# Kernel tuning notes

Hardware: AMD Instinct MI355X
Metric: run time of the kernel (lower is better)

Reference implementation:

```python
import jax, jax.numpy as jnp
import numpy as np

B, S, D = 8, 2048, 512

def setup_inputs() -> dict:
    key = jax.random.key(0)
    ks = jax.random.split(key, 9)
    scale = 1.0 / np.sqrt(D)
    return {
        "x": jax.random.normal(ks[0], (B, S, D), dtype=jnp.float32),
        "attention_mask": jax.random.uniform(ks[1], (B, S), dtype=jnp.float32),
        "Wq": jax.random.normal(ks[2], (D, D), dtype=jnp.float32) * scale,
        "bq": jax.random.normal(ks[3], (D,), dtype=jnp.float32) * 0.01,
        "Wk": jax.random.normal(ks[4], (D, D), dtype=jnp.float32) * scale,
        "bk": jax.random.normal(ks[5], (D,), dtype=jnp.float32) * 0.01,
        "Wv": jax.random.normal(ks[6], (D, D), dtype=jnp.float32) * scale,
        "bv": jax.random.normal(ks[7], (D,), dtype=jnp.float32) * 0.01,
    }

def reference(x, attention_mask, Wq, bq, Wk, bk, Wv, bv):
    # Single-head self-attention, full O(S^2) scores as in the original.
    q = jnp.einsum('bsd,df->bsf', x, Wq) + bq  # [B,S,D]
    k = jnp.einsum('bsd,df->bsf', x, Wk) + bk
    v = jnp.einsum('bsd,df->bsf', x, Wv) + bv
    scores = jnp.einsum('bqd,bkd->bqk', q, k) / jnp.sqrt(jnp.float32(D))  # [B,S,S]
    attn = jax.nn.softmax(scores, axis=2)
    weighted = jnp.einsum('bqk,bkd->bqd', attn, v)  # [B,S,D]
    # mask applied multiplicatively to the output, per original code
    return weighted * attention_mask[:, :, None]
```

## Files before the change

kernel.cpp:

```cpp
#include <hip/hip_runtime.h>
#include <math.h>
#include <stdint.h>


typedef _Float16 f16x8 __attribute__((ext_vector_type(8)));
typedef _Float16 f16x4 __attribute__((ext_vector_type(4)));
typedef _Float16 f16x2 __attribute__((ext_vector_type(2)));
typedef float f32x4 __attribute__((ext_vector_type(4)));

__device__ __forceinline__ void async16(const _Float16* g, _Float16* l) {
    __builtin_amdgcn_global_load_lds(
        (const __attribute__((address_space(1))) unsigned int*)(uintptr_t)g,
        (__attribute__((address_space(3))) unsigned int*)(unsigned int)(uintptr_t)l,
        16, 0, 0);
}

__device__ __forceinline__ float frag_sum8(f16x8 v, float acc) {
#if __has_builtin(__builtin_amdgcn_fdot2)
    const f16x2 one2 = {(_Float16)1.f, (_Float16)1.f};
    const f16x2* p = (const f16x2*)&v;
    acc = __builtin_amdgcn_fdot2(p[0], one2, acc, false);
    acc = __builtin_amdgcn_fdot2(p[1], one2, acc, false);
    acc = __builtin_amdgcn_fdot2(p[2], one2, acc, false);
    acc = __builtin_amdgcn_fdot2(p[3], one2, acc, false);
#else
#pragma unroll
    for (int j = 0; j < 8; j++) acc += (float)v[j];
#endif
    return acc;
}

template <bool WITH_RS>
__device__ __forceinline__ void mfma_gemm_core64(
    const _Float16* __restrict__ A, int lda,
    const _Float16* __restrict__ B, int ldb,
    int K, int row0, int col0,
    _Float16* As, _Float16* Bs, f32x4 acc[4][4], float rs[4])
{
    const int tid  = threadIdx.x;
    const int lane = tid & 63;
    const int wave = tid >> 6;
    const int wm   = wave >> 1, wn = wave & 1;

    const int rc  = lane >> 3;
    const int swz = ((lane & 7) ^ rc) * 8;

    const _Float16* gA[4]; const _Float16* gB[4];
    _Float16* lA[4]; _Float16* lB[4];
#pragma unroll
    for (int i = 0; i < 4; i++) {
        int c = wave * 4 + i;
        gA[i] = A + (size_t)(row0 + 8 * c + rc) * lda + swz;
        gB[i] = B + (size_t)(col0 + 8 * c + rc) * ldb + swz;
        lA[i] = As + c * 512;
        lB[i] = Bs + c * 512;
    }

    const int fr = lane & 15;
    const int q  = lane >> 4;
    const int fx = fr & 7;

    for (int k0 = 0; k0 < K; k0 += 64) {
        __syncthreads();
#pragma unroll
        for (int i = 0; i < 4; i++) {
            async16(gA[i] + k0, lA[i]);
            async16(gB[i] + k0, lB[i]);
        }
        __syncthreads();
#pragma unroll
        for (int step = 0; step < 2; step++) {
            f16x8 af[4], bf[4];
#pragma unroll
            for (int t = 0; t < 4; t++) {
                int ra = wm * 64 + t * 16 + fr;
                int rb = wn * 64 + t * 16 + fr;
                int kc = ((step * 4 + q) ^ fx) * 8;
                af[t] = *(const f16x8*)&As[ra * 64 + kc];
                bf[t] = *(const f16x8*)&Bs[rb * 64 + kc];
            }
            if (WITH_RS) {
#pragma unroll
                for (int t = 0; t < 4; t++) rs[t] = frag_sum8(af[t], rs[t]);
            }
#pragma unroll
            for (int tm = 0; tm < 4; tm++)
#pragma unroll
                for (int tn = 0; tn < 4; tn++)
                    acc[tm][tn] = __builtin_amdgcn_mfma_f32_16x16x32_f16(
                        af[tm], bf[tn], acc[tm][tn], 0, 0, 0);
        }
    }
}

__global__ __launch_bounds__(256) void prep(
    const float* __restrict__ x,
    const float* __restrict__ Wq, const float* __restrict__ Wk,
    const float* __restrict__ Wv,
    _Float16* __restrict__ Xh,
    _Float16* __restrict__ WqT, _Float16* __restrict__ WkT,
    _Float16* __restrict__ WvT)
{
    const int bid = blockIdx.x;
    if (bid < 8192) {
        int i = (bid * 256 + threadIdx.x) * 4;
        float4 v = *(const float4*)(x + i);
        f16x4 h;
        h.x = (_Float16)v.x; h.y = (_Float16)v.y;
        h.z = (_Float16)v.z; h.w = (_Float16)v.w;
        *(f16x4*)&Xh[i] = h;
    } else {
        int t = bid - 8192;
        int z = t >> 10;
        const float* W = (z == 0) ? Wq : (z == 1) ? Wk : Wv;
        _Float16* Wt   = (z == 0) ? WqT : (z == 1) ? WkT : WvT;
        int idx = (t & 1023) * 256 + threadIdx.x;
        int n = idx >> 9, k = idx & 511;
        Wt[idx] = (_Float16)W[k * 512 + n];
    }
}

__global__ __launch_bounds__(256) void proj_mfma(
    const _Float16* __restrict__ Xh,
    const _Float16* __restrict__ WqT, const float* __restrict__ bq,
    const _Float16* __restrict__ WkT, const float* __restrict__ bk,
    const _Float16* __restrict__ WvT, const float* __restrict__ bv,
    _Float16* __restrict__ Qh, _Float16* __restrict__ Kh,
    _Float16* __restrict__ Vt)
{
    __shared__ __align__(16) _Float16 smem[2 * 128 * 64];
    _Float16* As = smem;
    _Float16* Bs = smem + 128 * 64;

    const int z = blockIdx.z;
    f32x4 acc[4][4];
#pragma unroll
    for (int i = 0; i < 4; i++)
#pragma unroll
        for (int j = 0; j < 4; j++) acc[i][j] = (f32x4){0.f, 0.f, 0.f, 0.f};
    float rs_unused[4];

    const int lane = threadIdx.x & 63, wave = threadIdx.x >> 6;
    const int wm = wave >> 1, wn = wave & 1;
    const int er = (lane >> 4) * 4, ec = lane & 15;

    if (z < 2) {
        const _Float16* Wt = (z == 0) ? WqT : WkT;
        const float* bias  = (z == 0) ? bq : bk;
        _Float16* P        = (z == 0) ? Qh : Kh;
        const float sc     = (z == 0) ? 0.04419417382415922f : 1.0f;
        const int row0 = blockIdx.x * 128, col0 = blockIdx.y * 128;
        mfma_gemm_core64<false>(Xh, 512, Wt, 512, 512, row0, col0, As, Bs, acc,
                                rs_unused);
#pragma unroll
        for (int tm = 0; tm < 4; tm++)
#pragma unroll
            for (int tn = 0; tn < 4; tn++) {
                int col = col0 + wn * 64 + tn * 16 + ec;
                float bb = bias[col];
#pragma unroll
                for (int r = 0; r < 4; r++) {
                    int row = row0 + wm * 64 + tm * 16 + er + r;
                    P[(size_t)row * 512 + col] = (_Float16)((acc[tm][tn][r] + bb) * sc);
                }
            }
    } else {
        const int row0 = blockIdx.y * 128;
        const int col0 = blockIdx.x * 128;
        mfma_gemm_core64<false>(WvT, 512, Xh, 512, 512, row0, col0, As, Bs, acc,
                                rs_unused);
#pragma unroll
        for (int tm = 0; tm < 4; tm++)
#pragma unroll
            for (int tn = 0; tn < 4; tn++) {
                int col = col0 + wn * 64 + tn * 16 + ec;
                size_t obase = (size_t)(col >> 11) * (512 * 2048) + (col & 2047);
#pragma unroll
                for (int r = 0; r < 4; r++) {
                    int row = row0 + wm * 64 + tm * 16 + er + r;
                    Vt[obase + (size_t)row * 2048] = (_Float16)(acc[tm][tn][r] + bv[row]);
                }
            }
    }
}

__global__ __launch_bounds__(256) void scores_mfma(
    const _Float16* __restrict__ Qh, const _Float16* __restrict__ Kh,
    _Float16* __restrict__ Sh)
{
    __shared__ __align__(16) _Float16 smem[2 * 128 * 64];
    _Float16* As = smem;
    _Float16* Bs = smem + 128 * 64;
    const int bid = blockIdx.x;
    const int b   = bid & 7;
    const int rem = bid >> 3;
    const int col0 = (rem & 15) * 128;
    const int row0 = (rem >> 4) * 128;

    const _Float16* A = Qh + (size_t)b * 2048 * 512;
    const _Float16* B = Kh + (size_t)b * 2048 * 512;
    _Float16* S = Sh + (size_t)b * 2048 * 2048;

    f32x4 acc[4][4];
#pragma unroll
    for (int i = 0; i < 4; i++)
#pragma unroll
        for (int j = 0; j < 4; j++) acc[i][j] = (f32x4){0.f, 0.f, 0.f, 0.f};
    float rs_unused[4];

    mfma_gemm_core64<false>(A, 512, B, 512, 512, row0, col0, As, Bs, acc,
                            rs_unused);

    const int lane = threadIdx.x & 63, wave = threadIdx.x >> 6;
    const int wm = wave >> 1, wn = wave & 1;
    const int er = (lane >> 4) * 4, ec = lane & 15;
#pragma unroll
    for (int tm = 0; tm < 4; tm++)
#pragma unroll
        for (int tn = 0; tn < 4; tn++) {
            int col = col0 + wn * 64 + tn * 16 + ec;
#pragma unroll
            for (int r = 0; r < 4; r++) {
                int row = row0 + wm * 64 + tm * 16 + er + r;
                S[(size_t)row * 2048 + col] = (_Float16)__expf(acc[tm][tn][r]);
            }
        }
}

__global__ __launch_bounds__(256) void av_mfma(
    const _Float16* __restrict__ Sh, const _Float16* __restrict__ Vt,
    const float* __restrict__ mask, float* __restrict__ out)
{
    __shared__ __align__(16) _Float16 smem[2 * 128 * 64];
    __shared__ float l_s[128];
    _Float16* As = smem;
    _Float16* Bs = smem + 128 * 64;
    const int bid = blockIdx.x;
    const int b   = bid & 7;
    const int rem = bid >> 3;
    const int col0 = (rem & 3) * 128;
    const int row0 = (rem >> 2) * 128;

    const _Float16* A = Sh + (size_t)b * 2048 * 2048;
    const _Float16* B = Vt + (size_t)b * 512 * 2048;
    float* O = out + (size_t)b * 2048 * 512;
    const float* mk = mask + (size_t)b * 2048;

    f32x4 acc[4][4];
#pragma unroll
    for (int i = 0; i < 4; i++)
#pragma unroll
        for (int j = 0; j < 4; j++) acc[i][j] = (f32x4){0.f, 0.f, 0.f, 0.f};
    float rs[4] = {0.f, 0.f, 0.f, 0.f};

    mfma_gemm_core64<true>(A, 2048, B, 2048, 2048, row0, col0, As, Bs, acc, rs);

    const int lane = threadIdx.x & 63, wave = threadIdx.x >> 6;
    const int wm = wave >> 1, wn = wave & 1;
    const int er = (lane >> 4) * 4, ec = lane & 15;

#pragma unroll
    for (int t = 0; t < 4; t++) {
        rs[t] += __shfl_xor(rs[t], 16, 64);
        rs[t] += __shfl_xor(rs[t], 32, 64);
    }
    if (wn == 0 && lane < 16) {
#pragma unroll
        for (int t = 0; t < 4; t++) l_s[wm * 64 + t * 16 + lane] = rs[t];
    }
    __syncthreads();

#pragma unroll
    for (int tm = 0; tm < 4; tm++)
#pragma unroll
        for (int r = 0; r < 4; r++) {
            int lrow = wm * 64 + tm * 16 + er + r;
            int row = row0 + lrow;
            float s = mk[row] / l_s[lrow];
#pragma unroll
            for (int tn = 0; tn < 4; tn++) {
                int col = col0 + wn * 64 + tn * 16 + ec;
                O[(size_t)row * 512 + col] = acc[tm][tn][r] * s;
            }
        }
}

extern "C" void kernel_launch(void* const* d_in, const int* in_sizes, int n_in,
                              void* d_out, int out_size, void* d_ws, size_t ws_size,
                              hipStream_t stream) {
    const float* x    = (const float*)d_in[0];
    const float* mask = (const float*)d_in[1];
    const float* Wq   = (const float*)d_in[2];
    const float* bq   = (const float*)d_in[3];
    const float* Wk   = (const float*)d_in[4];
    const float* bk   = (const float*)d_in[5];
    const float* Wv   = (const float*)d_in[6];
    const float* bv   = (const float*)d_in[7];
    float* out = (float*)d_out;

    const size_t BSD = (size_t)8 * 2048 * 512;
    _Float16* base = (_Float16*)d_ws;
    _Float16* Qh  = base;
    _Float16* Kh  = Qh + BSD;
    _Float16* Vt  = Kh + BSD;
    _Float16* WqT = Vt + BSD;
    _Float16* WkT = WqT + 512 * 512;
    _Float16* WvT = WkT + 512 * 512;
    _Float16* Xh  = WvT + 512 * 512;
    _Float16* Sh  = Xh;

    dim3 blk(256);
    prep<<<dim3(8192 + 3 * 1024), blk, 0, stream>>>(
        x, Wq, Wk, Wv, Xh, WqT, WkT, WvT);
    proj_mfma<<<dim3(128, 4, 3), blk, 0, stream>>>(
        Xh, WqT, bq, WkT, bk, WvT, bv, Qh, Kh, Vt);
    scores_mfma<<<dim3(2048), blk, 0, stream>>>(Qh, Kh, Sh);
    av_mfma<<<dim3(512), blk, 0, stream>>>(Sh, Vt, mask, out);
}
```

Baseline: 220.8 us.

## Double-buffer LDS tiles in MFMA GEMM core to overlap loads with compute

The shared GEMM core now uses two LDS buffers, issuing async global-to-LDS loads for the next K tile before computing on the current one, and waits with explicit vmcnt counts instead of full syncthreads. LDS per block doubles to 64 KB, and l_s in av_mfma reuses the tile buffer after an added barrier. This hides global load latency behind the MFMA work in all three GEMM kernels, at the cost of halving how many blocks fit per CU in LDS and relying on hand-placed waitcnt and barriers being correct.

```diff
diff --git a/kernel.cpp b/kernel.cpp
--- a/kernel.cpp
+++ b/kernel.cpp
@@ -35,7 +35,7 @@
     const _Float16* __restrict__ A, int lda,
     const _Float16* __restrict__ B, int ldb,
     int K, int row0, int col0,
-    _Float16* As, _Float16* Bs, f32x4 acc[4][4], float rs[4])
+    _Float16* sm, f32x4 acc[4][4], float rs[4])
 {
     const int tid  = threadIdx.x;
     const int lane = tid & 63;
@@ -46,28 +46,45 @@
     const int swz = ((lane & 7) ^ rc) * 8;
 
     const _Float16* gA[4]; const _Float16* gB[4];
-    _Float16* lA[4]; _Float16* lB[4];
+    int lA[4], lB[4];
 #pragma unroll
     for (int i = 0; i < 4; i++) {
         int c = wave * 4 + i;
         gA[i] = A + (size_t)(row0 + 8 * c + rc) * lda + swz;
         gB[i] = B + (size_t)(col0 + 8 * c + rc) * ldb + swz;
-        lA[i] = As + c * 512;
-        lB[i] = Bs + c * 512;
+        lA[i] = c * 512;
+        lB[i] = 8192 + c * 512;
     }
 
     const int fr = lane & 15;
     const int q  = lane >> 4;
     const int fx = fr & 7;
 
-    for (int k0 = 0; k0 < K; k0 += 64) {
-        __syncthreads();
-#pragma unroll
-        for (int i = 0; i < 4; i++) {
-            async16(gA[i] + k0, lA[i]);
-            async16(gB[i] + k0, lB[i]);
+#pragma unroll
+    for (int i = 0; i < 4; i++) {
+        async16(gA[i], sm + lA[i]);
+        async16(gB[i], sm + lB[i]);
+    }
+
+    int cur = 0;
+    for (int k0 = 0;; k0 += 64) {
+        const bool more = (k0 + 64) < K;
+        if (more) {
+            const int nb = (cur ^ 1) * 16384;
+#pragma unroll
+            for (int i = 0; i < 4; i++) {
+                async16(gA[i] + k0 + 64, sm + nb + lA[i]);
+                async16(gB[i] + k0 + 64, sm + nb + lB[i]);
+            }
+            asm volatile("s_waitcnt vmcnt(8)" ::: "memory");
+        } else {
+            asm volatile("s_waitcnt vmcnt(0)" ::: "memory");
         }
-        __syncthreads();
+        __builtin_amdgcn_s_barrier();
+        asm volatile("" ::: "memory");
+
+        const _Float16* As = sm + cur * 16384;
+        const _Float16* Bs = As + 8192;
 #pragma unroll
         for (int step = 0; step < 2; step++) {
             f16x8 af[4], bf[4];
@@ -90,6 +107,10 @@
                     acc[tm][tn] = __builtin_amdgcn_mfma_f32_16x16x32_f16(
                         af[tm], bf[tn], acc[tm][tn], 0, 0, 0);
         }
+        asm volatile("" ::: "memory");
+        if (!more) break;
+        __builtin_amdgcn_s_barrier();
+        cur ^= 1;
     }
 }
 
@@ -128,9 +149,7 @@
     _Float16* __restrict__ Qh, _Float16* __restrict__ Kh,
     _Float16* __restrict__ Vt)
 {
-    __shared__ __align__(16) _Float16 smem[2 * 128 * 64];
-    _Float16* As = smem;
-    _Float16* Bs = smem + 128 * 64;
+    __shared__ __align__(16) _Float16 smem[4 * 128 * 64];
 
     const int z = blockIdx.z;
     f32x4 acc[4][4];
@@ -150,7 +169,7 @@
         _Float16* P        = (z == 0) ? Qh : Kh;
         const float sc     = (z == 0) ? 0.04419417382415922f : 1.0f;
         const int row0 = blockIdx.x * 128, col0 = blockIdx.y * 128;
-        mfma_gemm_core64<false>(Xh, 512, Wt, 512, 512, row0, col0, As, Bs, acc,
+        mfma_gemm_core64<false>(Xh, 512, Wt, 512, 512, row0, col0, smem, acc,
                                 rs_unused);
 #pragma unroll
         for (int tm = 0; tm < 4; tm++)
@@ -167,7 +186,7 @@
     } else {
         const int row0 = blockIdx.y * 128;
         const int col0 = blockIdx.x * 128;
-        mfma_gemm_core64<false>(WvT, 512, Xh, 512, 512, row0, col0, As, Bs, acc,
+        mfma_gemm_core64<false>(WvT, 512, Xh, 512, 512, row0, col0, smem, acc,
                                 rs_unused);
 #pragma unroll
         for (int tm = 0; tm < 4; tm++)
@@ -188,9 +207,7 @@
     const _Float16* __restrict__ Qh, const _Float16* __restrict__ Kh,
     _Float16* __restrict__ Sh)
 {
-    __shared__ __align__(16) _Float16 smem[2 * 128 * 64];
-    _Float16* As = smem;
-    _Float16* Bs = smem + 128 * 64;
+    __shared__ __align__(16) _Float16 smem[4 * 128 * 64];
     const int bid = blockIdx.x;
     const int b   = bid & 7;
     const int rem = bid >> 3;
@@ -208,7 +225,7 @@
         for (int j = 0; j < 4; j++) acc[i][j] = (f32x4){0.f, 0.f, 0.f, 0.f};
     float rs_unused[4];
 
-    mfma_gemm_core64<false>(A, 512, B, 512, 512, row0, col0, As, Bs, acc,
+    mfma_gemm_core64<false>(A, 512, B, 512, 512, row0, col0, smem, acc,
                             rs_unused);
 
     const int lane = threadIdx.x & 63, wave = threadIdx.x >> 6;
@@ -231,10 +248,7 @@
     const _Float16* __restrict__ Sh, const _Float16* __restrict__ Vt,
     const float* __restrict__ mask, float* __restrict__ out)
 {
-    __shared__ __align__(16) _Float16 smem[2 * 128 * 64];
-    __shared__ float l_s[128];
-    _Float16* As = smem;
-    _Float16* Bs = smem + 128 * 64;
+    __shared__ __align__(16) _Float16 smem[4 * 128 * 64];
     const int bid = blockIdx.x;
     const int b   = bid & 7;
     const int rem = bid >> 3;
@@ -253,7 +267,7 @@
         for (int j = 0; j < 4; j++) acc[i][j] = (f32x4){0.f, 0.f, 0.f, 0.f};
     float rs[4] = {0.f, 0.f, 0.f, 0.f};
 
-    mfma_gemm_core64<true>(A, 2048, B, 2048, 2048, row0, col0, As, Bs, acc, rs);
+    mfma_gemm_core64<true>(A, 2048, B, 2048, 2048, row0, col0, smem, acc, rs);
 
     const int lane = threadIdx.x & 63, wave = threadIdx.x >> 6;
     const int wm = wave >> 1, wn = wave & 1;
@@ -264,6 +278,8 @@
         rs[t] += __shfl_xor(rs[t], 16, 64);
         rs[t] += __shfl_xor(rs[t], 32, 64);
     }
+    __syncthreads();
+    float* l_s = (float*)smem;
     if (wn == 0 && lane < 16) {
 #pragma unroll
         for (int t = 0; t < 4; t++) l_s[wm * 64 + t * 16 + lane] = rs[t];
```

Result: slower. 234.2 us (+6.1%).
